# Kernel tuning notes

Measured on AMD Instinct MI355X. Metric: run time of the kernel, lower is better.

Reference implementation:

```python
import jax, jax.numpy as jnp
import numpy as np

# Qwen3-Next GatedDeltaNet dims
H = 2048          # hidden_size
HK = 16           # linear_num_key_heads
HV = 32           # linear_num_value_heads
DK = 128          # linear_key_head_dim
DV = 128          # linear_value_head_dim
KDIM = HK * DK    # 2048
VDIM = HV * DV    # 4096
CONV_DIM = 2 * KDIM + VDIM  # 8192
KSIZE = 4         # linear_conv_kernel_dim
KV_RATIO = HV // HK
EPS = 1e-6        # rms_norm_eps
T = 1024


def setup_inputs() -> dict:
    key = jax.random.key(0)
    ks = jax.random.split(key, 8)
    s = lambda k, shape, sc=0.02: jax.random.normal(k, shape, jnp.float32) * sc
    return dict(
        hidden_states=jax.random.normal(ks[0], (1, T, H), jnp.float32),
        W_qkvz=s(ks[1], (H, 2 * KDIM + 2 * VDIM)),
        W_ba=s(ks[2], (H, 2 * HV)),
        conv_w=s(ks[3], (CONV_DIM, KSIZE), 0.2),   # depthwise, no bias
        dt_bias=jax.random.normal(ks[4], (HV,), jnp.float32) * 0.1,
        A_log=jnp.log(jax.random.uniform(ks[5], (HV,), jnp.float32, minval=1e-2, maxval=16.0)),
        norm_w=jnp.ones((DV,), jnp.float32),
        W_out=s(ks[6], (VDIM, H)),
    )


def _l2norm(x):
    # fla l2norm: x / sqrt(sum(x^2) + eps)
    return x * jax.lax.rsqrt(jnp.sum(x * x, axis=-1, keepdims=True) + 1e-6)


def reference(hidden_states, W_qkvz, W_ba, conv_w, dt_bias, A_log, norm_w, W_out):
    B, Tn, _ = hidden_states.shape
    qkvz = hidden_states @ W_qkvz                       # [B,T,2K+2V]
    ba = hidden_states @ W_ba                           # [B,T,2*HV]

    # fix_query_key_value_ordering: per k-head interleaved layout
    qkvz = qkvz.reshape(B, Tn, HK, 2 * DK + 2 * KV_RATIO * DV)
    q = qkvz[..., :DK]                                  # [B,T,HK,DK]
    k = qkvz[..., DK:2 * DK]
    v = qkvz[..., 2 * DK:2 * DK + KV_RATIO * DV].reshape(B, Tn, HV, DV)
    z = qkvz[..., 2 * DK + KV_RATIO * DV:].reshape(B, Tn, HV, DV)
    ba = ba.reshape(B, Tn, HK, 2 * KV_RATIO)
    b = ba[..., :KV_RATIO].reshape(B, Tn, HV)
    a = ba[..., KV_RATIO:].reshape(B, Tn, HV)

    # causal depthwise conv1d (no bias) + silu, single contiguous sequence
    mixed = jnp.concatenate([q.reshape(B, Tn, KDIM), k.reshape(B, Tn, KDIM),
                             v.reshape(B, Tn, VDIM)], axis=-1)   # [B,T,C]
    x = mixed.transpose(0, 2, 1)                                   # [B,C,T]
    x = jnp.pad(x, ((0, 0), (0, 0), (KSIZE - 1, 0)))
    y = jax.lax.conv_general_dilated(x, conv_w[:, None, :], (1,), 'VALID',
                                     feature_group_count=CONV_DIM)
    y = jax.nn.silu(y).transpose(0, 2, 1)                          # [B,T,C]
    q = y[..., :KDIM].reshape(B, Tn, HK, DK)
    k = y[..., KDIM:2 * KDIM].reshape(B, Tn, HK, DK)
    v = y[..., 2 * KDIM:].reshape(B, Tn, HV, DV)

    beta = jax.nn.sigmoid(b)                                       # [B,T,HV]
    g = -jnp.exp(A_log) * jax.nn.softplus(a + dt_bias)             # [B,T,HV] (log decay)

    # qk l2norm in kernel + fla default scale on q; GQA head repeat
    q = jnp.repeat(_l2norm(q), KV_RATIO, axis=2) * (DK ** -0.5)    # [B,T,HV,DK]
    k = jnp.repeat(_l2norm(k), KV_RATIO, axis=2)

    def scan_one(qs, ks, vs, gs, bs):
        def step(S, inp):
            qt, kt, vt, gt, bt = inp                    # per-head slices
            S = S * jnp.exp(gt)[:, None, None]          # gated decay, [HV,DK,DV]
            kv = jnp.einsum('hk,hkv->hv', kt, S)        # current memory readout
            delta = (vt - kv) * bt[:, None]             # delta rule with beta gate
            S = S + kt[:, :, None] * delta[:, None, :]
            o = jnp.einsum('hk,hkv->hv', qt, S)
            return S, o
        S0 = jnp.zeros((HV, DK, DV), qs.dtype)
        _, out = jax.lax.scan(step, S0, (qs, ks, vs, gs, bs))
        return out                                      # [T,HV,DV]

    core = jax.vmap(scan_one)(q, k, v, g, beta)         # [B,T,HV,DV]

    # gated RMSNorm per value head: x*silu(z) then rmsnorm, then weight
    gated = core * jax.nn.silu(z)
    gated = gated * jax.lax.rsqrt(jnp.mean(gated * gated, axis=-1, keepdims=True) + EPS)
    gated = gated * norm_w

    return gated.reshape(B, Tn, VDIM) @ W_out           # [B,T,H]
```

## Files before the change

### kernel.cpp

```cpp
#include <hip/hip_runtime.h>
#include <hip/hip_bf16.h>
#include <math.h>


#define T_LEN 1024
#define HK_N 16
#define HV_N 32
#define NQKVZ 12288
#define CHUNK 64
#define NCHUNK 16

typedef __bf16 bf16x8 __attribute__((ext_vector_type(8)));
typedef float f32x4 __attribute__((ext_vector_type(4)));

__device__ __forceinline__ ushort4 pack4(const f32x4 v) {
  ushort4 o;
  o.x = __bfloat16_as_ushort(__float2bfloat16(v[0]));
  o.y = __bfloat16_as_ushort(__float2bfloat16(v[1]));
  o.z = __bfloat16_as_ushort(__float2bfloat16(v[2]));
  o.w = __bfloat16_as_ushort(__float2bfloat16(v[3]));
  return o;
}

template <int BM, bool BF16OUT>
__global__ __launch_bounds__(256) void gemm_bf16(const __hip_bfloat16* __restrict__ A,
                                                 const __hip_bfloat16* __restrict__ B,
                                                 void* __restrict__ Cv,
                                                 int M, int N, int Klen, int ldk) {
  constexpr int AITS = BM / 32;
  constexpr int MF = BM / 32;
  __shared__ __align__(16) __hip_bfloat16 As[2][BM * 64];
  __shared__ __align__(16) __hip_bfloat16 Bs[2][128 * 64];
  const int tid = threadIdx.x;
  const int wid = tid >> 6, lane = tid & 63;
  const int wr = wid >> 1, wc = wid & 1;
  const int m0 = blockIdx.y * BM, n0 = blockIdx.x * 128;
  const size_t kbase = (size_t)blockIdx.z * Klen;
  const int lrow = lane & 15, lk = lane >> 4;
  const int rswz = (lrow & 7) * 8;
  f32x4 acc[MF][4] = {};
  const int nk = Klen >> 6;

#define GSTAGE(b_, k0_) do {                                                    \
    _Pragma("unroll") for (int it = 0; it < AITS; ++it) {                       \
      const int c_ = it * 256 + tid;                                            \
      const int row_ = c_ >> 3;                                                 \
      const int col8_ = ((c_ & 7) ^ (row_ & 7)) * 8;                            \
      __builtin_amdgcn_global_load_lds(                                         \
          (const __attribute__((address_space(1))) void*)                       \
              (A + (size_t)(m0 + row_) * ldk + kbase + (k0_) + col8_),          \
          (__attribute__((address_space(3))) void*)(&As[b_][it * 2048 + tid * 8]), 16, 0, 0); \
    }                                                                           \
    _Pragma("unroll") for (int it = 0; it < 4; ++it) {                          \
      const int c_ = it * 256 + tid;                                            \
      const int row_ = c_ >> 3;                                                 \
      const int col8_ = ((c_ & 7) ^ (row_ & 7)) * 8;                            \
      __builtin_amdgcn_global_load_lds(                                         \
          (const __attribute__((address_space(1))) void*)                       \
              (B + (size_t)(n0 + row_) * ldk + kbase + (k0_) + col8_),          \
          (__attribute__((address_space(3))) void*)(&Bs[b_][it * 2048 + tid * 8]), 16, 0, 0); \
    }                                                                           \
  } while (0)

  GSTAGE(0, 0);
  int buf = 0;
  for (int k = 0; k < nk; ++k) {
    if (k + 1 < nk) {
      GSTAGE(buf ^ 1, (k + 1) << 6);
      if constexpr (BM == 128) asm volatile("s_waitcnt vmcnt(8)" ::: "memory");
      else                     asm volatile("s_waitcnt vmcnt(6)" ::: "memory");
    } else {
      asm volatile("s_waitcnt vmcnt(0)" ::: "memory");
    }
    __builtin_amdgcn_s_barrier();
    __builtin_amdgcn_sched_barrier(0);
#pragma unroll
    for (int kk = 0; kk < 2; ++kk) {
      bf16x8 af[MF], bfv[4];
#pragma unroll
      for (int m = 0; m < MF; ++m)
        af[m] = *reinterpret_cast<const bf16x8*>(
            &As[buf][(wr * (BM / 2) + m * 16 + lrow) * 64 + ((kk * 32 + lk * 8) ^ rswz)]);
#pragma unroll
      for (int n = 0; n < 4; ++n)
        bfv[n] = *reinterpret_cast<const bf16x8*>(
            &Bs[buf][(wc * 64 + n * 16 + lrow) * 64 + ((kk * 32 + lk * 8) ^ rswz)]);
#pragma unroll
      for (int m = 0; m < MF; ++m)
#pragma unroll
        for (int n = 0; n < 4; ++n)
          acc[m][n] = __builtin_amdgcn_mfma_f32_16x16x32_bf16(af[m], bfv[n], acc[m][n], 0, 0, 0);
    }
    __builtin_amdgcn_sched_barrier(0);
    __builtin_amdgcn_s_barrier();
    buf ^= 1;
  }
#undef GSTAGE
  if constexpr (BF16OUT) {
    __hip_bfloat16* Cz = (__hip_bfloat16*)Cv + (size_t)blockIdx.z * M * N;
#pragma unroll
    for (int m = 0; m < MF; ++m)
#pragma unroll
      for (int n = 0; n < 4; ++n)
#pragma unroll
        for (int r = 0; r < 4; ++r)
          Cz[(size_t)(m0 + wr * (BM / 2) + m * 16 + lk * 4 + r) * N + n0 + wc * 64 + n * 16 + lrow] =
              __float2bfloat16(acc[m][n][r]);
  } else {
    float* Cz = (float*)Cv + (size_t)blockIdx.z * M * N;
#pragma unroll
    for (int m = 0; m < MF; ++m)
#pragma unroll
      for (int n = 0; n < 4; ++n)
#pragma unroll
        for (int r = 0; r < 4; ++r)
          Cz[(size_t)(m0 + wr * (BM / 2) + m * 16 + lk * 4 + r) * N + n0 + wc * 64 + n * 16 + lrow] =
              acc[m][n][r];
  }
}

__global__ void add4(const __hip_bfloat16* __restrict__ P, float* __restrict__ out, int n) {
  const int i = (blockIdx.x * 256 + threadIdx.x) * 4;
  if (i < n) {
    float s[4] = {0.f, 0.f, 0.f, 0.f};
#pragma unroll
    for (int z = 0; z < 4; ++z) {
      const ushort4 v = *reinterpret_cast<const ushort4*>(P + (size_t)z * n + i);
      s[0] += __bfloat162float(__ushort_as_bfloat16(v.x));
      s[1] += __bfloat162float(__ushort_as_bfloat16(v.y));
      s[2] += __bfloat162float(__ushort_as_bfloat16(v.z));
      s[3] += __bfloat162float(__ushort_as_bfloat16(v.w));
    }
    *reinterpret_cast<float4*>(out + i) = make_float4(s[0], s[1], s[2], s[3]);
  }
}

__global__ __launch_bounds__(256) void prep2(const float* __restrict__ X,
                                             __hip_bfloat16* __restrict__ Xb,
                                             const float* __restrict__ Wq,
                                             __hip_bfloat16* __restrict__ Wqt,
                                             const float* __restrict__ Wba,
                                             float* __restrict__ P) {
  __shared__ __align__(16) float smem[16 * 512];
  const int bid = blockIdx.x;
  const int tid = threadIdx.x;
  if (bid < 2048) {
    const int i = (bid * 256 + tid) * 4;
    const float4 v = *reinterpret_cast<const float4*>(X + i);
    ushort4 o;
    o.x = __bfloat16_as_ushort(__float2bfloat16(v.x));
    o.y = __bfloat16_as_ushort(__float2bfloat16(v.y));
    o.z = __bfloat16_as_ushort(__float2bfloat16(v.z));
    o.w = __bfloat16_as_ushort(__float2bfloat16(v.w));
    *reinterpret_cast<ushort4*>((void*)(Xb + i)) = o;
  } else if (bid < 8192) {
    float (*tl)[65] = reinterpret_cast<float (*)[65]>(smem);
    const int b = bid - 2048;
    const int n0 = (b % 192) * 64, k0 = (b / 192) * 64;
    const int N = NQKVZ, K = 2048;
    const int rc = tid & 15, rr = tid >> 4;
#pragma unroll
    for (int i = 0; i < 4; ++i) {
      const int k = rr + 16 * i;
      const float4 v = *reinterpret_cast<const float4*>(&Wq[(size_t)(k0 + k) * N + n0 + rc * 4]);
      tl[k][rc * 4 + 0] = v.x;
      tl[k][rc * 4 + 1] = v.y;
      tl[k][rc * 4 + 2] = v.z;
      tl[k][rc * 4 + 3] = v.w;
    }
    __syncthreads();
    const int wcx = tid & 7, wry = tid >> 3;
#pragma unroll
    for (int i = 0; i < 2; ++i) {
      const int n = wry + 32 * i;
      uint u[8];
#pragma unroll
      for (int j = 0; j < 8; ++j)
        u[j] = __bfloat16_as_ushort(__float2bfloat16(tl[wcx * 8 + j][n]));
      uint4 o;
      o.x = u[0] | (u[1] << 16);
      o.y = u[2] | (u[3] << 16);
      o.z = u[4] | (u[5] << 16);
      o.w = u[6] | (u[7] << 16);
      *reinterpret_cast<uint4*>((void*)&Wqt[(size_t)(n0 + n) * K + k0 + wcx * 8]) = o;
    }
  } else {
    float (*Xs)[512] = reinterpret_cast<float (*)[512]>(smem);
    const int b = bid - 8192;
    const int tt = b & 63, ks = b >> 6;
    const int c = tid & 63, r4 = tid >> 6;
    const float* xsrc = X + (size_t)(tt * 16) * 2048 + ks * 512;
#pragma unroll
    for (int u = 0; u < 8; ++u) {
      const int flat = (u * 256 + tid) * 4;
      const int r = flat >> 9, k = flat & 511;
      *reinterpret_cast<float4*>(&Xs[r][k]) =
          *reinterpret_cast<const float4*>(&xsrc[(size_t)r * 2048 + k]);
    }
    __syncthreads();
    float acc[4] = {};
    const float* wp = Wba + (size_t)(ks * 512) * 64 + c;
    for (int k = 0; k < 512; k += 8) {
      float w[8];
#pragma unroll
      for (int u = 0; u < 8; ++u) w[u] = wp[(size_t)(k + u) * 64];
#pragma unroll
      for (int u = 0; u < 8; ++u)
#pragma unroll
        for (int i = 0; i < 4; ++i)
          acc[i] = fmaf(Xs[r4 * 4 + i][k + u], w[u], acc[i]);
    }
    float* pp = P + ((size_t)ks * 1024 + tt * 16 + r4 * 4) * 64 + c;
#pragma unroll
    for (int i = 0; i < 4; ++i) pp[(size_t)i * 64] = acc[i];
  }
}

__global__ __launch_bounds__(256) void convs(const __hip_bfloat16* __restrict__ qkvz,
                                             const float* __restrict__ conv_w,
                                             float* __restrict__ QK,
                                             float* __restrict__ V,
                                             const float* __restrict__ P,
                                             const float* __restrict__ dt_bias,
                                             const float* __restrict__ A_log,
                                             float* __restrict__ gg,
                                             float* __restrict__ bet) {
  const int bid = blockIdx.x;
  const int tid = threadIdx.x;
  if (bid < 4096) {
    const int kh = bid & 15;
    const int t = (bid >> 4) * 4 + (tid >> 6);
    const int l = tid & 63;
    const int cols[4] = {kh * 768 + l, kh * 768 + l + 64,
                         kh * 768 + 128 + l, kh * 768 + 128 + l + 64};
    const int chs[4] = {kh * 128 + l, kh * 128 + l + 64,
                        2048 + kh * 128 + l, 2048 + kh * 128 + l + 64};
    float y[4];
#pragma unroll
    for (int j = 0; j < 4; ++j) {
      const float* wp = &conv_w[chs[j] * 4];
      float acc = 0.f;
#pragma unroll
      for (int s = 0; s < 4; ++s) {
        const int tt = t - 3 + s;
        if (tt >= 0)
          acc = fmaf(__bfloat162float(qkvz[(size_t)tt * NQKVZ + cols[j]]), wp[s], acc);
      }
      y[j] = acc / (1.f + expf(-acc));
    }
    float sq = y[0] * y[0] + y[1] * y[1];
    float sk = y[2] * y[2] + y[3] * y[3];
#pragma unroll
    for (int off = 32; off; off >>= 1) {
      sq += __shfl_xor(sq, off);
      sk += __shfl_xor(sk, off);
    }
    const float rq = rsqrtf(sq + 1e-6f) * 0.08838834764831845f;
    const float rk = rsqrtf(sk + 1e-6f);
    const size_t qb = (size_t)t * 4096 + kh * 128;
    QK[qb + l] = y[0] * rq;
    QK[qb + l + 64] = y[1] * rq;
    QK[qb + 2048 + l] = y[2] * rk;
    QK[qb + 2048 + l + 64] = y[3] * rk;
  } else if (bid < 4608) {
    const int b = bid - 4096;
    const int c2 = (b & 15) * 256 + tid;
    const int vh = c2 >> 7;
    const int col = (vh >> 1) * 768 + 256 + (vh & 1) * 128 + (c2 & 127);
    const int t0 = (b >> 4) * 32;
    const float4 w = *reinterpret_cast<const float4*>(&conv_w[(4096 + c2) * 4]);
    float x0, x1, x2;
    if (t0 == 0) {
      x0 = 0.f; x1 = 0.f; x2 = 0.f;
    } else {
      x0 = __bfloat162float(qkvz[(size_t)(t0 - 3) * NQKVZ + col]);
      x1 = __bfloat162float(qkvz[(size_t)(t0 - 2) * NQKVZ + col]);
      x2 = __bfloat162float(qkvz[(size_t)(t0 - 1) * NQKVZ + col]);
    }
#pragma unroll 4
    for (int tt = 0; tt < 32; ++tt) {
      const int t = t0 + tt;
      const float x3 = __bfloat162float(qkvz[(size_t)t * NQKVZ + col]);
      float acc = x0 * w.x;
      acc = fmaf(x1, w.y, acc);
      acc = fmaf(x2, w.z, acc);
      acc = fmaf(x3, w.w, acc);
      V[(size_t)t * 4096 + c2] = acc / (1.f + expf(-acc));
      x0 = x1; x1 = x2; x2 = x3;
    }
  } else {
    const int idx = (bid - 4608) * 256 + tid;
    const int t = idx >> 5, vh = idx & 31;
    const int cb = (vh >> 1) * 4 + (vh & 1);
    float b = 0.f, a = 0.f;
#pragma unroll
    for (int s = 0; s < 4; ++s) {
      b += P[((size_t)s * 1024 + t) * 64 + cb];
      a += P[((size_t)s * 1024 + t) * 64 + cb + 2];
    }
    const float x = a + dt_bias[vh];
    const float sp = (x > 20.f) ? x : log1pf(expf(x));
    gg[idx] = -expf(A_log[vh]) * sp;
    bet[idx] = 1.f / (1.f + expf(-b));
  }
}

__global__ __launch_bounds__(256, 2) void phase1(
    const float* __restrict__ QK, const float* __restrict__ V,
    const float* __restrict__ g, const float* __restrict__ bet,
    __hip_bfloat16* __restrict__ Ub, __hip_bfloat16* __restrict__ Wb,
    __hip_bfloat16* __restrict__ KTb, __hip_bfloat16* __restrict__ Qgb,
    __hip_bfloat16* __restrict__ Bb, float* __restrict__ gend) {
  const int vh = blockIdx.x, ch = blockIdx.y, kh = vh >> 1;
  const int tid = threadIdx.x;
  const int t0 = ch * CHUNK;
  __shared__ __align__(16) __hip_bfloat16 KbS[64][128];
  __shared__ __align__(16) __hip_bfloat16 QbS[64][128];
  __shared__ __align__(16) float Al[64][68];
  __shared__ float bs[64], gams[64], bets[64], lams[64];

  const int row = tid >> 2;
  const size_t hb = (size_t)ch * 32 + vh;
  {
    const int cc = (tid & 3) * 32;
    const float* ksrc = &QK[(size_t)(t0 + row) * 4096 + 2048 + kh * 128 + cc];
    const float* qsrc = &QK[(size_t)(t0 + row) * 4096 + kh * 128 + cc];
#pragma unroll
    for (int u = 0; u < 32; u += 4) {
      const float4 kv = *reinterpret_cast<const float4*>(ksrc + u);
      const float4 qv = *reinterpret_cast<const float4*>(qsrc + u);
      const int d0 = cc + u;
      const int sidx = (d0 & 7) | ((((d0 >> 3) ^ (row & 7)) & 15) << 3);
      ushort4 kk4, qq4;
      kk4.x = __bfloat16_as_ushort(__float2bfloat16(kv.x));
      kk4.y = __bfloat16_as_ushort(__float2bfloat16(kv.y));
      kk4.z = __bfloat16_as_ushort(__float2bfloat16(kv.z));
      kk4.w = __bfloat16_as_ushort(__float2bfloat16(kv.w));
      qq4.x = __bfloat16_as_ushort(__float2bfloat16(qv.x));
      qq4.y = __bfloat16_as_ushort(__float2bfloat16(qv.y));
      qq4.z = __bfloat16_as_ushort(__float2bfloat16(qv.z));
      qq4.w = __bfloat16_as_ushort(__float2bfloat16(qv.w));
      *reinterpret_cast<ushort4*>(&KbS[row][sidx]) = kk4;
      *reinterpret_cast<ushort4*>(&QbS[row][sidx]) = qq4;
    }
  }
  if (tid < 64) {
    float b = g[(size_t)(t0 + tid) * 32 + vh];
#pragma unroll
    for (int off = 1; off < 64; off <<= 1) {
      const float o = __shfl_up(b, off);
      if (tid >= off) b += o;
    }
    const float b63 = __shfl(b, 63);
    const float ga = expf(b);
    bs[tid] = b;
    gams[tid] = ga;
    lams[tid] = expf(b63 - b);
    bets[tid] = bet[(size_t)(t0 + tid) * 32 + vh];
    if (tid == 63) gend[ch * 32 + vh] = ga;
  }
  __syncthreads();
  {
    const int i = tid & 63;
    const float li = lams[i];
    __hip_bfloat16* kt = &KTb[hb * 128 * 64];
    const int dbase = (tid >> 6) * 32;
#pragma unroll
    for (int dd = 0; dd < 32; ++dd) {
      const int d = dbase + dd;
      const int sidx = (d & 7) | ((((d >> 3) ^ (i & 7)) & 15) << 3);
      kt[(size_t)d * 64 + (i ^ ((d & 7) << 3))] =
          __float2bfloat16(li * __bfloat162float(KbS[i][sidx]));
    }
  }
  {
    const float gai = gams[row];
    __hip_bfloat16* qg = &Qgb[(hb * 64 + row) * 128];
    const int cc = (tid & 3) * 32;
#pragma unroll
    for (int u = 0; u < 32; u += 4) {
      const int d0 = cc + u;
      const int sidx = (d0 & 7) | ((((d0 >> 3) ^ (row & 7)) & 15) << 3);
      ushort4 qq;
      qq.x = __bfloat16_as_ushort(__float2bfloat16(gai * __bfloat162float(QbS[row][sidx + 0])));
      qq.y = __bfloat16_as_ushort(__float2bfloat16(gai * __bfloat162float(QbS[row][sidx + 1])));
      qq.z = __bfloat16_as_ushort(__float2bfloat16(gai * __bfloat162float(QbS[row][sidx + 2])));
      qq.w = __bfloat16_as_ushort(__float2bfloat16(gai * __bfloat162float(QbS[row][sidx + 3])));
      *reinterpret_cast<ushort4*>(&qg[d0 ^ ((row & 7) << 3)]) = qq;
    }
  }
  {
    const int w = tid >> 6, lane = tid & 63;
    const int lrow = lane & 15, lk = lane >> 4;
    bf16x8 af[4], qf[4];
#pragma unroll
    for (int kk = 0; kk < 4; ++kk) {
      const int c = ((kk * 4 + lk) ^ (lrow & 7)) * 8;
      af[kk] = *reinterpret_cast<const bf16x8*>(&KbS[w * 16 + lrow][c]);
      qf[kk] = *reinterpret_cast<const bf16x8*>(&QbS[w * 16 + lrow][c]);
    }
#pragma unroll
    for (int n = 0; n < 4; ++n) {
      f32x4 aA = {}, aB = {};
#pragma unroll
      for (int kk = 0; kk < 4; ++kk) {
        const bf16x8 bf = *reinterpret_cast<const bf16x8*>(
            &KbS[n * 16 + lrow][((kk * 4 + lk) ^ (lrow & 7)) * 8]);
        aA = __builtin_amdgcn_mfma_f32_16x16x32_bf16(af[kk], bf, aA, 0, 0, 0);
        aB = __builtin_amdgcn_mfma_f32_16x16x32_bf16(qf[kk], bf, aB, 0, 0, 0);
      }
      __hip_bfloat16* Bout = &Bb[hb * 64 * 64];
#pragma unroll
      for (int r = 0; r < 4; ++r) {
        const int i = w * 16 + lk * 4 + r;
        const int j = n * 16 + lrow;
        const float dec = expf(bs[i] - bs[j]);
        Al[i][j] = (j < i) ? bets[i] * dec * aA[r] : 0.f;
        Bout[(size_t)i * 64 + (j ^ ((i & 7) << 3))] =
            __float2bfloat16((j <= i) ? dec * aB[r] : 0.f);
      }
    }
  }
  __syncthreads();
  {
    const int cc = tid;
    float x[64];
    const bool isV = cc < 128;
    const float* src = isV ? &V[(size_t)t0 * 4096 + vh * 128 + cc]
                           : &QK[(size_t)t0 * 4096 + 2048 + kh * 128 + (cc - 128)];
#pragma unroll
    for (int i = 0; i < 64; ++i) {
      const float sc = isV ? bets[i] : bets[i] * gams[i];
      x[i] = sc * src[(size_t)i * 4096];
    }
#pragma unroll
    for (int i = 1; i < 64; ++i) {
      float s0 = 0.f, s1 = 0.f, s2 = 0.f, s3 = 0.f;
      int j = 0;
#pragma unroll
      for (; j + 4 <= i; j += 4) {
        const float4 a = *reinterpret_cast<const float4*>(&Al[i][j]);
        s0 = fmaf(a.x, x[j], s0);
        s1 = fmaf(a.y, x[j + 1], s1);
        s2 = fmaf(a.z, x[j + 2], s2);
        s3 = fmaf(a.w, x[j + 3], s3);
      }
#pragma unroll
      for (; j < i; ++j) s0 = fmaf(Al[i][j], x[j], s0);
      x[i] -= (s0 + s1) + (s2 + s3);
    }
    if (isV) {
      __hip_bfloat16* dst = &Ub[hb * 64 * 128 + cc];
#pragma unroll
      for (int i = 0; i < 64; ++i) dst[(size_t)i * 128] = __float2bfloat16(x[i]);
    } else {
      const int d = cc - 128;
      __hip_bfloat16* dst = &Wb[hb * 64 * 128];
#pragma unroll
      for (int i = 0; i < 64; ++i)
        dst[(size_t)i * 128 + (d ^ ((i & 7) << 3))] = __float2bfloat16(-x[i]);
    }
  }
}

__global__ __launch_bounds__(128) void phaseB(
    const __hip_bfloat16* __restrict__ Ug, const __hip_bfloat16* __restrict__ Wb,
    const __hip_bfloat16* __restrict__ KTb, const __hip_bfloat16* __restrict__ Qgb,
    const __hip_bfloat16* __restrict__ Bb, const float* __restrict__ gendg,
    float* __restrict__ Og) {
  const int vh = blockIdx.x, slice = blockIdx.y;
  const int tid = threadIdx.x, lane = tid & 63, w = tid >> 6;
  const int l15 = lane & 15, l4 = lane >> 4;
  const int cg = slice * 32 + w * 16;
  const int swz = (l15 & 7) << 3;

  __shared__ __hip_bfloat16 Wl[2][8192];
  __shared__ __hip_bfloat16 KTl[2][8192];
  __shared__ __hip_bfloat16 Qgl[2][8192];
  __shared__ __hip_bfloat16 Bl[2][4096];
  __shared__ __hip_bfloat16 Sop[2][2048];
  __shared__ __hip_bfloat16 dLs[2][1024];

  f32x4 accS[8] = {};
  for (int x = lane; x < 1024; x += 64) reinterpret_cast<uint*>(Sop[w])[x] = 0;

  float ubuf[4][4];
#define STAGE(b_, c_) do {                                                      \
    const size_t hb_ = ((size_t)(c_) * 32 + vh);                                \
    _Pragma("unroll") for (int it = 0; it < 8; ++it) {                          \
      __builtin_amdgcn_global_load_lds(                                         \
          (const __attribute__((address_space(1))) void*)(Wb + hb_ * 8192 + it * 1024 + tid * 8), \
          (__attribute__((address_space(3))) void*)(&Wl[b_][it * 1024 + tid * 8]), 16, 0, 0); \
      __builtin_amdgcn_global_load_lds(                                         \
          (const __attribute__((address_space(1))) void*)(KTb + hb_ * 8192 + it * 1024 + tid * 8), \
          (__attribute__((address_space(3))) void*)(&KTl[b_][it * 1024 + tid * 8]), 16, 0, 0); \
      __builtin_amdgcn_global_load_lds(                                         \
          (const __attribute__((address_space(1))) void*)(Qgb + hb_ * 8192 + it * 1024 + tid * 8), \
          (__attribute__((address_space(3))) void*)(&Qgl[b_][it * 1024 + tid * 8]), 16, 0, 0); \
      if (it < 4)                                                               \
        __builtin_amdgcn_global_load_lds(                                       \
            (const __attribute__((address_space(1))) void*)(Bb + hb_ * 4096 + it * 1024 + tid * 8), \
            (__attribute__((address_space(3))) void*)(&Bl[b_][it * 1024 + tid * 8]), 16, 0, 0); \
    }                                                                           \
  } while (0)
#define UPREF(c_) do {                                                          \
    const __hip_bfloat16* up_ = Ug + ((size_t)(c_) * 32 + vh) * 64 * 128 + cg + l15; \
    _Pragma("unroll") for (int m_ = 0; m_ < 4; ++m_)                            \
      _Pragma("unroll") for (int r_ = 0; r_ < 4; ++r_)                          \
        ubuf[m_][r_] = __bfloat162float(up_[(size_t)(m_ * 16 + l4 * 4 + r_) * 128]); \
  } while (0)

  STAGE(0, 0);
  UPREF(0);
  __syncthreads();
  int buf = 0;
  for (int ch = 0; ch < NCHUNK; ++ch) {
    if (ch + 1 < NCHUNK) STAGE(buf ^ 1, ch + 1);
    f32x4 acc_d[4];
#pragma unroll
    for (int m = 0; m < 4; ++m) {
      f32x4 t;
      t[0] = ubuf[m][0]; t[1] = ubuf[m][1]; t[2] = ubuf[m][2]; t[3] = ubuf[m][3];
      acc_d[m] = t;
    }
    if (ch + 1 < NCHUNK) UPREF(ch + 1);
#pragma unroll
    for (int t = 0; t < 4; ++t) {
      const bf16x8 bS = *reinterpret_cast<const bf16x8*>(
          &Sop[w][l15 * 128 + ((t * 32 + l4 * 8) ^ swz)]);
#pragma unroll
      for (int m = 0; m < 4; ++m) {
        const bf16x8 aW = *reinterpret_cast<const bf16x8*>(
            &Wl[buf][(m * 16 + l15) * 128 + ((t * 32 + l4 * 8) ^ swz)]);
        acc_d[m] = __builtin_amdgcn_mfma_f32_16x16x32_bf16(aW, bS, acc_d[m], 0, 0, 0);
      }
    }
#pragma unroll
    for (int m = 0; m < 4; ++m)
      *reinterpret_cast<ushort4*>(&dLs[w][l15 * 64 + ((m * 16 + l4 * 4) ^ swz)]) =
          pack4(acc_d[m]);
    f32x4 acc_o[4] = {};
#pragma unroll
    for (int t = 0; t < 4; ++t) {
      const bf16x8 bS = *reinterpret_cast<const bf16x8*>(
          &Sop[w][l15 * 128 + ((t * 32 + l4 * 8) ^ swz)]);
#pragma unroll
      for (int m = 0; m < 4; ++m) {
        const bf16x8 aQ = *reinterpret_cast<const bf16x8*>(
            &Qgl[buf][(m * 16 + l15) * 128 + ((t * 32 + l4 * 8) ^ swz)]);
        acc_o[m] = __builtin_amdgcn_mfma_f32_16x16x32_bf16(aQ, bS, acc_o[m], 0, 0, 0);
      }
    }
#pragma unroll
    for (int t2 = 0; t2 < 2; ++t2) {
      const bf16x8 bD = *reinterpret_cast<const bf16x8*>(
          &dLs[w][l15 * 64 + ((t2 * 32 + l4 * 8) ^ swz)]);
#pragma unroll
      for (int m = 0; m < 4; ++m) {
        const bf16x8 aB = *reinterpret_cast<const bf16x8*>(
            &Bl[buf][(m * 16 + l15) * 64 + ((t2 * 32 + l4 * 8) ^ swz)]);
        acc_o[m] = __builtin_amdgcn_mfma_f32_16x16x32_bf16(aB, bD, acc_o[m], 0, 0, 0);
      }
    }
    float* ob = Og + (size_t)(ch * 64) * 4096 + (size_t)vh * 128 + cg + l15;
#pragma unroll
    for (int m = 0; m < 4; ++m)
#pragma unroll
      for (int r = 0; r < 4; ++r)
        ob[(size_t)(m * 16 + l4 * 4 + r) * 4096] = acc_o[m][r];
    const float ge = gendg[ch * 32 + vh];
#pragma unroll
    for (int f = 0; f < 8; ++f) {
      accS[f][0] *= ge; accS[f][1] *= ge; accS[f][2] *= ge; accS[f][3] *= ge;
    }
#pragma unroll
    for (int t2 = 0; t2 < 2; ++t2) {
      const bf16x8 bD = *reinterpret_cast<const bf16x8*>(
          &dLs[w][l15 * 64 + ((t2 * 32 + l4 * 8) ^ swz)]);
#pragma unroll
      for (int f = 0; f < 8; ++f) {
        const bf16x8 aK = *reinterpret_cast<const bf16x8*>(
            &KTl[buf][(f * 16 + l15) * 64 + ((t2 * 32 + l4 * 8) ^ swz)]);
        accS[f] = __builtin_amdgcn_mfma_f32_16x16x32_bf16(aK, bD, accS[f], 0, 0, 0);
      }
    }
#pragma unroll
    for (int f = 0; f < 8; ++f)
      *reinterpret_cast<ushort4*>(&Sop[w][l15 * 128 + ((f * 16 + l4 * 4) ^ swz)]) =
          pack4(accS[f]);
    __syncthreads();
    buf ^= 1;
  }
#undef STAGE
#undef UPREF
}

__global__ __launch_bounds__(256) void gfuse(const float* __restrict__ O,
                                             const __hip_bfloat16* __restrict__ qkvz,
                                             const float* __restrict__ norm_w,
                                             __hip_bfloat16* __restrict__ G,
                                             const float* __restrict__ Wo,
                                             __hip_bfloat16* __restrict__ Wot) {
  __shared__ float tl[64][65];
  const int bid = blockIdx.x;
  const int tid = threadIdx.x;
  if (bid < 8192) {
    const int vh = (bid & 7) * 4 + (tid >> 6);
    const int t = bid >> 3, l = tid & 63;
    const size_t ob = (size_t)t * 4096 + vh * 128;
    const size_t zb = (size_t)t * NQKVZ + (vh >> 1) * 768 + 512 + (vh & 1) * 128;
    const float o0 = O[ob + l], o1 = O[ob + l + 64];
    const float z0 = __bfloat162float(qkvz[zb + l]);
    const float z1 = __bfloat162float(qkvz[zb + l + 64]);
    const float g0 = o0 * z0 / (1.f + expf(-z0));
    const float g1 = o1 * z1 / (1.f + expf(-z1));
    float ss = g0 * g0 + g1 * g1;
#pragma unroll
    for (int off = 32; off; off >>= 1) ss += __shfl_xor(ss, off);
    const float rr = rsqrtf(ss * (1.f / 128.f) + 1e-6f);
    G[ob + l] = __float2bfloat16(g0 * rr * norm_w[l]);
    G[ob + l + 64] = __float2bfloat16(g1 * rr * norm_w[l + 64]);
    return;
  }
  const int b = bid - 8192;
  const int n0 = (b & 31) * 64, k0 = (b >> 5) * 64;
  const int N = 2048, K = 4096;
  const int rc = tid & 15, rr2 = tid >> 4;
#pragma unroll
  for (int i = 0; i < 4; ++i) {
    const int k = rr2 + 16 * i;
    const float4 v = *reinterpret_cast<const float4*>(&Wo[(size_t)(k0 + k) * N + n0 + rc * 4]);
    tl[k][rc * 4 + 0] = v.x;
    tl[k][rc * 4 + 1] = v.y;
    tl[k][rc * 4 + 2] = v.z;
    tl[k][rc * 4 + 3] = v.w;
  }
  __syncthreads();
  const int wcx = tid & 7, wry = tid >> 3;
#pragma unroll
  for (int i = 0; i < 2; ++i) {
    const int n = wry + 32 * i;
    uint u[8];
#pragma unroll
    for (int j = 0; j < 8; ++j)
      u[j] = __bfloat16_as_ushort(__float2bfloat16(tl[wcx * 8 + j][n]));
    uint4 o;
    o.x = u[0] | (u[1] << 16);
    o.y = u[2] | (u[3] << 16);
    o.z = u[4] | (u[5] << 16);
    o.w = u[6] | (u[7] << 16);
    *reinterpret_cast<uint4*>((void*)&Wot[(size_t)(n0 + n) * K + k0 + wcx * 8]) = o;
  }
}

extern "C" void kernel_launch(void* const* d_in, const int* in_sizes, int n_in,
                              void* d_out, int out_size, void* d_ws, size_t ws_size,
                              hipStream_t stream) {
  const float* X = (const float*)d_in[0];
  const float* W_qkvz = (const float*)d_in[1];
  const float* W_ba = (const float*)d_in[2];
  const float* conv_w = (const float*)d_in[3];
  const float* dt_bias = (const float*)d_in[4];
  const float* A_log = (const float*)d_in[5];
  const float* norm_w = (const float*)d_in[6];
  const float* W_out = (const float*)d_in[7];
  float* out = (float*)d_out;

  float* ws = (float*)d_ws;
  float* qkvz = ws;
  float* P = qkvz + (size_t)T_LEN * NQKVZ;
  float* QK = P + 262144;
  float* V = QK + (size_t)T_LEN * 4096;
  float* U_f = V + (size_t)T_LEN * 4096;
  float* Wb_f = U_f + (size_t)NCHUNK * 32 * 64 * 128;
  float* KT_f = Wb_f + 2097152;
  float* Qg_f = KT_f + 2097152;
  float* Bb_f = Qg_f + 2097152;
  float* gg = Bb_f + 1048576;
  float* bet = gg + 32768;
  float* gend = bet + 32768;

  __hip_bfloat16* qkvzb = (__hip_bfloat16*)qkvz;
  __hip_bfloat16* Ub = (__hip_bfloat16*)U_f;
  __hip_bfloat16* Wb = (__hip_bfloat16*)Wb_f;
  __hip_bfloat16* KTb = (__hip_bfloat16*)KT_f;
  __hip_bfloat16* Qgb = (__hip_bfloat16*)Qg_f;
  __hip_bfloat16* Bb = (__hip_bfloat16*)Bb_f;
  __hip_bfloat16* Wqkvz_t = (__hip_bfloat16*)V;
  __hip_bfloat16* Xb = (__hip_bfloat16*)Qg_f;
  __hip_bfloat16* Gb = (__hip_bfloat16*)Bb_f;
  __hip_bfloat16* Wout_t = (__hip_bfloat16*)qkvz;
  float* O = V;
  __hip_bfloat16* Pout = (__hip_bfloat16*)U_f;

  prep2<<<dim3(2048 + 6144 + 256), 256, 0, stream>>>(X, Xb, W_qkvz, Wqkvz_t, W_ba, P);
  gemm_bf16<128, true><<<dim3(NQKVZ / 128, T_LEN / 128, 1), 256, 0, stream>>>(
      Xb, Wqkvz_t, qkvzb, T_LEN, NQKVZ, 2048, 2048);
  convs<<<dim3(4096 + 512 + 128), 256, 0, stream>>>(qkvzb, conv_w, QK, V, P,
                                                    dt_bias, A_log, gg, bet);
  phase1<<<dim3(HV_N, NCHUNK), 256, 0, stream>>>(QK, V, gg, bet, Ub, Wb, KTb, Qgb, Bb, gend);
  phaseB<<<dim3(HV_N, 4), 128, 0, stream>>>(Ub, Wb, KTb, Qgb, Bb, gend, O);
  gfuse<<<dim3(8192 + 2048), 256, 0, stream>>>(O, qkvzb, norm_w, Gb, W_out, Wout_t);
  gemm_bf16<128, true><<<dim3(2048 / 128, T_LEN / 128, 4), 256, 0, stream>>>(
      Gb, Wout_t, Pout, T_LEN, 2048, 1024, 4096);
  add4<<<dim3(T_LEN * 2048 / 4 / 256), 256, 0, stream>>>(Pout, out, T_LEN * 2048);
}
```

Measured before the change: 265.0 us.

## Add 256x256-tile 512-thread GEMM for QKVZ projection with direct-to-LDS loads

Adds a dedicated bf16 MFMA GEMM kernel with 256x256 output tiles and 8 waves. It uses global_load_lds direct-to-LDS double buffering, an XOR swizzle, and split-K-half fragment loads, and routes the large QKVZ projection through it. The bigger tile raises arithmetic intensity and cuts redundant global traffic. In exchange the grid shrinks to 48*4=192 blocks, which may underfill the GPU's CUs. It also uses large LDS (128KB) and many accumulator registers, limiting occupancy.

```diff
diff --git a/kernel.cpp b/kernel.cpp
--- a/kernel.cpp
+++ b/kernel.cpp
@@ -20,6 +20,99 @@
   o.z = __bfloat16_as_ushort(__float2bfloat16(v[2]));
   o.w = __bfloat16_as_ushort(__float2bfloat16(v[3]));
   return o;
+}
+
+__global__ __launch_bounds__(512) void gemm256(const __hip_bfloat16* __restrict__ A,
+                                               const __hip_bfloat16* __restrict__ B,
+                                               __hip_bfloat16* __restrict__ C,
+                                               int M, int N, int Klen) {
+  __shared__ __align__(16) __hip_bfloat16 As[2][256 * 64];
+  __shared__ __align__(16) __hip_bfloat16 Bs[2][256 * 64];
+  const int tid = threadIdx.x;
+  const int wid = tid >> 6, lane = tid & 63;
+  const int wr = wid >> 2, wc = wid & 3;
+  const int m0 = blockIdx.y * 256, n0 = blockIdx.x * 256;
+  const int lrow = lane & 15, lk = lane >> 4;
+  const int rswz = (lrow & 7) * 8;
+  f32x4 acc[8][4] = {};
+  const int nk = Klen >> 6;
+
+#define GST(b_, kt_) do {                                                       \
+    _Pragma("unroll") for (int it = 0; it < 4; ++it) {                          \
+      const int c_ = it * 512 + tid;                                            \
+      const int row_ = c_ >> 3;                                                 \
+      const int col8_ = ((c_ & 7) ^ (row_ & 7)) * 8;                            \
+      __builtin_amdgcn_global_load_lds(                                         \
+          (const __attribute__((address_space(1))) void*)                       \
+              (A + (size_t)(m0 + row_) * Klen + ((kt_) << 6) + col8_),          \
+          (__attribute__((address_space(3))) void*)(&As[b_][c_ * 8]), 16, 0, 0);\
+    }                                                                           \
+    _Pragma("unroll") for (int it = 0; it < 4; ++it) {                          \
+      const int c_ = it * 512 + tid;                                            \
+      const int row_ = c_ >> 3;                                                 \
+      const int col8_ = ((c_ & 7) ^ (row_ & 7)) * 8;                            \
+      __builtin_amdgcn_global_load_lds(                                         \
+          (const __attribute__((address_space(1))) void*)                       \
+              (B + (size_t)(n0 + row_) * Klen + ((kt_) << 6) + col8_),          \
+          (__attribute__((address_space(3))) void*)(&Bs[b_][c_ * 8]), 16, 0, 0);\
+    }                                                                           \
+  } while (0)
+
+  GST(0, 0);
+  GST(1, 1);
+  int cur = 0;
+  for (int t = 0; t < nk; ++t) {
+    if (t < nk - 1) asm volatile("s_waitcnt vmcnt(8)" ::: "memory");
+    else            asm volatile("s_waitcnt vmcnt(0)" ::: "memory");
+    __builtin_amdgcn_s_barrier();
+    __builtin_amdgcn_sched_barrier(0);
+    bf16x8 af[8], bfv[4];
+#pragma unroll
+    for (int m = 0; m < 8; ++m)
+      af[m] = *reinterpret_cast<const bf16x8*>(
+          &As[cur][(wr * 128 + m * 16 + lrow) * 64 + ((lk * 8) ^ rswz)]);
+#pragma unroll
+    for (int n = 0; n < 4; ++n)
+      bfv[n] = *reinterpret_cast<const bf16x8*>(
+          &Bs[cur][(wc * 64 + n * 16 + lrow) * 64 + ((lk * 8) ^ rswz)]);
+    __builtin_amdgcn_s_setprio(1);
+#pragma unroll
+    for (int m = 0; m < 8; ++m)
+#pragma unroll
+      for (int n = 0; n < 4; ++n)
+        acc[m][n] = __builtin_amdgcn_mfma_f32_16x16x32_bf16(af[m], bfv[n], acc[m][n], 0, 0, 0);
+    __builtin_amdgcn_s_setprio(0);
+#pragma unroll
+    for (int m = 0; m < 8; ++m)
+      af[m] = *reinterpret_cast<const bf16x8*>(
+          &As[cur][(wr * 128 + m * 16 + lrow) * 64 + ((32 + lk * 8) ^ rswz)]);
+#pragma unroll
+    for (int n = 0; n < 4; ++n)
+      bfv[n] = *reinterpret_cast<const bf16x8*>(
+          &Bs[cur][(wc * 64 + n * 16 + lrow) * 64 + ((32 + lk * 8) ^ rswz)]);
+    asm volatile("s_waitcnt lgkmcnt(0)" ::: "memory");
+    __builtin_amdgcn_sched_barrier(0);
+    __builtin_amdgcn_s_barrier();
+    __builtin_amdgcn_sched_barrier(0);
+    if (t + 2 < nk) GST(cur, t + 2);
+    __builtin_amdgcn_s_setprio(1);
+#pragma unroll
+    for (int m = 0; m < 8; ++m)
+#pragma unroll
+      for (int n = 0; n < 4; ++n)
+        acc[m][n] = __builtin_amdgcn_mfma_f32_16x16x32_bf16(af[m], bfv[n], acc[m][n], 0, 0, 0);
+    __builtin_amdgcn_s_setprio(0);
+    cur ^= 1;
+  }
+#undef GST
+#pragma unroll
+  for (int m = 0; m < 8; ++m)
+#pragma unroll
+    for (int n = 0; n < 4; ++n)
+#pragma unroll
+      for (int r = 0; r < 4; ++r)
+        C[(size_t)(m0 + wr * 128 + m * 16 + lk * 4 + r) * N + n0 + wc * 64 + n * 16 + lrow] =
+            __float2bfloat16(acc[m][n][r]);
 }
 
 template <int BM, bool BF16OUT>
@@ -694,8 +787,8 @@
   __hip_bfloat16* Pout = (__hip_bfloat16*)U_f;
 
   prep2<<<dim3(2048 + 6144 + 256), 256, 0, stream>>>(X, Xb, W_qkvz, Wqkvz_t, W_ba, P);
-  gemm_bf16<128, true><<<dim3(NQKVZ / 128, T_LEN / 128, 1), 256, 0, stream>>>(
-      Xb, Wqkvz_t, qkvzb, T_LEN, NQKVZ, 2048, 2048);
+  gemm256<<<dim3(NQKVZ / 256, T_LEN / 256), 512, 0, stream>>>(
+      Xb, Wqkvz_t, qkvzb, T_LEN, NQKVZ, 2048);
   convs<<<dim3(4096 + 512 + 128), 256, 0, stream>>>(qkvzb, conv_w, QK, V, P,
                                                     dt_bias, A_log, gg, bet);
   phase1<<<dim3(HV_N, NCHUNK), 256, 0, stream>>>(QK, V, gg, bet, Ub, Wb, KTb, Qgb, Bb, gend);
```

Result: faster. 251.4 us, median of 2 (-5.1%).

## Use 256x256 GEMM tiles with prefetch-two pipeline and deeper split-K

Applied to the files above, without the earlier changes.

Replaces the 128-tile bf16 GEMM with a 512-thread kernel that computes 256x256 output tiles. It prefetches the tile two K-steps ahead and interleaves the LDS fragment reads for the second K-half with MFMA work, raising wave priority during the MFMA sections. The output projection moves from 4-way to 8-way split-K, with an 8-input reduction kernel. The weight transpose also becomes its own kernel, separate from the X cast and the small b/a projection. Larger tiles give more operand reuse per byte loaded, but the QKVZ GEMM now launches only 192 workgroups, which may leave CUs idle. The doubled split-K partial buffer also adds memory traffic.

```diff
diff --git a/kernel.cpp b/kernel.cpp
--- a/kernel.cpp
+++ b/kernel.cpp
@@ -22,109 +22,107 @@
   return o;
 }
 
-template <int BM, bool BF16OUT>
-__global__ __launch_bounds__(256) void gemm_bf16(const __hip_bfloat16* __restrict__ A,
-                                                 const __hip_bfloat16* __restrict__ B,
-                                                 void* __restrict__ Cv,
-                                                 int M, int N, int Klen, int ldk) {
-  constexpr int AITS = BM / 32;
-  constexpr int MF = BM / 32;
-  __shared__ __align__(16) __hip_bfloat16 As[2][BM * 64];
-  __shared__ __align__(16) __hip_bfloat16 Bs[2][128 * 64];
+__global__ __launch_bounds__(512) void gemm256(const __hip_bfloat16* __restrict__ A,
+                                               const __hip_bfloat16* __restrict__ B,
+                                               __hip_bfloat16* __restrict__ C,
+                                               int M, int N, int Klen, int ldk) {
+  __shared__ __align__(16) __hip_bfloat16 As[2][256 * 64];
+  __shared__ __align__(16) __hip_bfloat16 Bs[2][256 * 64];
   const int tid = threadIdx.x;
   const int wid = tid >> 6, lane = tid & 63;
-  const int wr = wid >> 1, wc = wid & 1;
-  const int m0 = blockIdx.y * BM, n0 = blockIdx.x * 128;
+  const int wr = wid >> 2, wc = wid & 3;
+  const int m0 = blockIdx.y * 256, n0 = blockIdx.x * 256;
   const size_t kbase = (size_t)blockIdx.z * Klen;
+  __hip_bfloat16* Cz = C + (size_t)blockIdx.z * M * N;
   const int lrow = lane & 15, lk = lane >> 4;
   const int rswz = (lrow & 7) * 8;
-  f32x4 acc[MF][4] = {};
+  f32x4 acc[8][4] = {};
   const int nk = Klen >> 6;
 
-#define GSTAGE(b_, k0_) do {                                                    \
-    _Pragma("unroll") for (int it = 0; it < AITS; ++it) {                       \
-      const int c_ = it * 256 + tid;                                            \
+#define GST(b_, kt_) do {                                                       \
+    _Pragma("unroll") for (int it = 0; it < 4; ++it) {                          \
+      const int c_ = it * 512 + tid;                                            \
       const int row_ = c_ >> 3;                                                 \
       const int col8_ = ((c_ & 7) ^ (row_ & 7)) * 8;                            \
       __builtin_amdgcn_global_load_lds(                                         \
           (const __attribute__((address_space(1))) void*)                       \
-              (A + (size_t)(m0 + row_) * ldk + kbase + (k0_) + col8_),          \
-          (__attribute__((address_space(3))) void*)(&As[b_][it * 2048 + tid * 8]), 16, 0, 0); \
+              (A + (size_t)(m0 + row_) * ldk + kbase + ((kt_) << 6) + col8_),   \
+          (__attribute__((address_space(3))) void*)(&As[b_][c_ * 8]), 16, 0, 0);\
     }                                                                           \
     _Pragma("unroll") for (int it = 0; it < 4; ++it) {                          \
-      const int c_ = it * 256 + tid;                                            \
+      const int c_ = it * 512 + tid;                                            \
       const int row_ = c_ >> 3;                                                 \
       const int col8_ = ((c_ & 7) ^ (row_ & 7)) * 8;                            \
       __builtin_amdgcn_global_load_lds(                                         \
           (const __attribute__((address_space(1))) void*)                       \
-              (B + (size_t)(n0 + row_) * ldk + kbase + (k0_) + col8_),          \
-          (__attribute__((address_space(3))) void*)(&Bs[b_][it * 2048 + tid * 8]), 16, 0, 0); \
+              (B + (size_t)(n0 + row_) * ldk + kbase + ((kt_) << 6) + col8_),   \
+          (__attribute__((address_space(3))) void*)(&Bs[b_][c_ * 8]), 16, 0, 0);\
     }                                                                           \
   } while (0)
 
-  GSTAGE(0, 0);
-  int buf = 0;
-  for (int k = 0; k < nk; ++k) {
-    if (k + 1 < nk) {
-      GSTAGE(buf ^ 1, (k + 1) << 6);
-      if constexpr (BM == 128) asm volatile("s_waitcnt vmcnt(8)" ::: "memory");
-      else                     asm volatile("s_waitcnt vmcnt(6)" ::: "memory");
-    } else {
-      asm volatile("s_waitcnt vmcnt(0)" ::: "memory");
-    }
+  GST(0, 0);
+  GST(1, 1);
+  int cur = 0;
+  for (int t = 0; t < nk; ++t) {
+    if (t < nk - 1) asm volatile("s_waitcnt vmcnt(8)" ::: "memory");
+    else            asm volatile("s_waitcnt vmcnt(0)" ::: "memory");
     __builtin_amdgcn_s_barrier();
     __builtin_amdgcn_sched_barrier(0);
-#pragma unroll
-    for (int kk = 0; kk < 2; ++kk) {
-      bf16x8 af[MF], bfv[4];
-#pragma unroll
-      for (int m = 0; m < MF; ++m)
-        af[m] = *reinterpret_cast<const bf16x8*>(
-            &As[buf][(wr * (BM / 2) + m * 16 + lrow) * 64 + ((kk * 32 + lk * 8) ^ rswz)]);
+    bf16x8 af[8], bfv[4];
+#pragma unroll
+    for (int m = 0; m < 8; ++m)
+      af[m] = *reinterpret_cast<const bf16x8*>(
+          &As[cur][(wr * 128 + m * 16 + lrow) * 64 + ((lk * 8) ^ rswz)]);
+#pragma unroll
+    for (int n = 0; n < 4; ++n)
+      bfv[n] = *reinterpret_cast<const bf16x8*>(
+          &Bs[cur][(wc * 64 + n * 16 + lrow) * 64 + ((lk * 8) ^ rswz)]);
+    __builtin_amdgcn_s_setprio(1);
+#pragma unroll
+    for (int m = 0; m < 8; ++m)
 #pragma unroll
       for (int n = 0; n < 4; ++n)
-        bfv[n] = *reinterpret_cast<const bf16x8*>(
-            &Bs[buf][(wc * 64 + n * 16 + lrow) * 64 + ((kk * 32 + lk * 8) ^ rswz)]);
-#pragma unroll
-      for (int m = 0; m < MF; ++m)
-#pragma unroll
-        for (int n = 0; n < 4; ++n)
-          acc[m][n] = __builtin_amdgcn_mfma_f32_16x16x32_bf16(af[m], bfv[n], acc[m][n], 0, 0, 0);
-    }
+        acc[m][n] = __builtin_amdgcn_mfma_f32_16x16x32_bf16(af[m], bfv[n], acc[m][n], 0, 0, 0);
+    __builtin_amdgcn_s_setprio(0);
+#pragma unroll
+    for (int m = 0; m < 8; ++m)
+      af[m] = *reinterpret_cast<const bf16x8*>(
+          &As[cur][(wr * 128 + m * 16 + lrow) * 64 + ((32 + lk * 8) ^ rswz)]);
+#pragma unroll
+    for (int n = 0; n < 4; ++n)
+      bfv[n] = *reinterpret_cast<const bf16x8*>(
+          &Bs[cur][(wc * 64 + n * 16 + lrow) * 64 + ((32 + lk * 8) ^ rswz)]);
+    asm volatile("s_waitcnt lgkmcnt(0)" ::: "memory");
     __builtin_amdgcn_sched_barrier(0);
     __builtin_amdgcn_s_barrier();
-    buf ^= 1;
-  }
-#undef GSTAGE
-  if constexpr (BF16OUT) {
-    __hip_bfloat16* Cz = (__hip_bfloat16*)Cv + (size_t)blockIdx.z * M * N;
-#pragma unroll
-    for (int m = 0; m < MF; ++m)
+    __builtin_amdgcn_sched_barrier(0);
+    if (t + 2 < nk) GST(cur, t + 2);
+    __builtin_amdgcn_s_setprio(1);
+#pragma unroll
+    for (int m = 0; m < 8; ++m)
 #pragma unroll
       for (int n = 0; n < 4; ++n)
-#pragma unroll
-        for (int r = 0; r < 4; ++r)
-          Cz[(size_t)(m0 + wr * (BM / 2) + m * 16 + lk * 4 + r) * N + n0 + wc * 64 + n * 16 + lrow] =
-              __float2bfloat16(acc[m][n][r]);
-  } else {
-    float* Cz = (float*)Cv + (size_t)blockIdx.z * M * N;
-#pragma unroll
-    for (int m = 0; m < MF; ++m)
-#pragma unroll
-      for (int n = 0; n < 4; ++n)
-#pragma unroll
-        for (int r = 0; r < 4; ++r)
-          Cz[(size_t)(m0 + wr * (BM / 2) + m * 16 + lk * 4 + r) * N + n0 + wc * 64 + n * 16 + lrow] =
-              acc[m][n][r];
-  }
-}
-
-__global__ void add4(const __hip_bfloat16* __restrict__ P, float* __restrict__ out, int n) {
+        acc[m][n] = __builtin_amdgcn_mfma_f32_16x16x32_bf16(af[m], bfv[n], acc[m][n], 0, 0, 0);
+    __builtin_amdgcn_s_setprio(0);
+    cur ^= 1;
+  }
+#undef GST
+#pragma unroll
+  for (int m = 0; m < 8; ++m)
+#pragma unroll
+    for (int n = 0; n < 4; ++n)
+#pragma unroll
+      for (int r = 0; r < 4; ++r)
+        Cz[(size_t)(m0 + wr * 128 + m * 16 + lk * 4 + r) * N + n0 + wc * 64 + n * 16 + lrow] =
+            __float2bfloat16(acc[m][n][r]);
+}
+
+__global__ void add8(const __hip_bfloat16* __restrict__ P, float* __restrict__ out, int n) {
   const int i = (blockIdx.x * 256 + threadIdx.x) * 4;
   if (i < n) {
     float s[4] = {0.f, 0.f, 0.f, 0.f};
 #pragma unroll
-    for (int z = 0; z < 4; ++z) {
+    for (int z = 0; z < 8; ++z) {
       const ushort4 v = *reinterpret_cast<const ushort4*>(P + (size_t)z * n + i);
       s[0] += __bfloat162float(__ushort_as_bfloat16(v.x));
       s[1] += __bfloat162float(__ushort_as_bfloat16(v.y));
@@ -135,13 +133,11 @@
   }
 }
 
-__global__ __launch_bounds__(256) void prep2(const float* __restrict__ X,
+__global__ __launch_bounds__(256) void preba(const float* __restrict__ X,
                                              __hip_bfloat16* __restrict__ Xb,
-                                             const float* __restrict__ Wq,
-                                             __hip_bfloat16* __restrict__ Wqt,
                                              const float* __restrict__ Wba,
                                              float* __restrict__ P) {
-  __shared__ __align__(16) float smem[16 * 512];
+  __shared__ __align__(16) float Xs[16][512];
   const int bid = blockIdx.x;
   const int tid = threadIdx.x;
   if (bid < 2048) {
@@ -153,40 +149,8 @@
     o.z = __bfloat16_as_ushort(__float2bfloat16(v.z));
     o.w = __bfloat16_as_ushort(__float2bfloat16(v.w));
     *reinterpret_cast<ushort4*>((void*)(Xb + i)) = o;
-  } else if (bid < 8192) {
-    float (*tl)[65] = reinterpret_cast<float (*)[65]>(smem);
+  } else {
     const int b = bid - 2048;
-    const int n0 = (b % 192) * 64, k0 = (b / 192) * 64;
-    const int N = NQKVZ, K = 2048;
-    const int rc = tid & 15, rr = tid >> 4;
-#pragma unroll
-    for (int i = 0; i < 4; ++i) {
-      const int k = rr + 16 * i;
-      const float4 v = *reinterpret_cast<const float4*>(&Wq[(size_t)(k0 + k) * N + n0 + rc * 4]);
-      tl[k][rc * 4 + 0] = v.x;
-      tl[k][rc * 4 + 1] = v.y;
-      tl[k][rc * 4 + 2] = v.z;
-      tl[k][rc * 4 + 3] = v.w;
-    }
-    __syncthreads();
-    const int wcx = tid & 7, wry = tid >> 3;
-#pragma unroll
-    for (int i = 0; i < 2; ++i) {
-      const int n = wry + 32 * i;
-      uint u[8];
-#pragma unroll
-      for (int j = 0; j < 8; ++j)
-        u[j] = __bfloat16_as_ushort(__float2bfloat16(tl[wcx * 8 + j][n]));
-      uint4 o;
-      o.x = u[0] | (u[1] << 16);
-      o.y = u[2] | (u[3] << 16);
-      o.z = u[4] | (u[5] << 16);
-      o.w = u[6] | (u[7] << 16);
-      *reinterpret_cast<uint4*>((void*)&Wqt[(size_t)(n0 + n) * K + k0 + wcx * 8]) = o;
-    }
-  } else {
-    float (*Xs)[512] = reinterpret_cast<float (*)[512]>(smem);
-    const int b = bid - 8192;
     const int tt = b & 63, ks = b >> 6;
     const int c = tid & 63, r4 = tid >> 6;
     const float* xsrc = X + (size_t)(tt * 16) * 2048 + ks * 512;
@@ -213,6 +177,41 @@
     float* pp = P + ((size_t)ks * 1024 + tt * 16 + r4 * 4) * 64 + c;
 #pragma unroll
     for (int i = 0; i < 4; ++i) pp[(size_t)i * 64] = acc[i];
+  }
+}
+
+__global__ __launch_bounds__(256) void wtrans(const float* __restrict__ Wq,
+                                              __hip_bfloat16* __restrict__ Wqt) {
+  __shared__ float tl[64][65];
+  const int b = blockIdx.x;
+  const int n0 = (b % 192) * 64, k0 = (b / 192) * 64;
+  const int N = NQKVZ, K = 2048;
+  const int tid = threadIdx.x;
+  const int rc = tid & 15, rr = tid >> 4;
+#pragma unroll
+  for (int i = 0; i < 4; ++i) {
+    const int k = rr + 16 * i;
+    const float4 v = *reinterpret_cast<const float4*>(&Wq[(size_t)(k0 + k) * N + n0 + rc * 4]);
+    tl[k][rc * 4 + 0] = v.x;
+    tl[k][rc * 4 + 1] = v.y;
+    tl[k][rc * 4 + 2] = v.z;
+    tl[k][rc * 4 + 3] = v.w;
+  }
+  __syncthreads();
+  const int wcx = tid & 7, wry = tid >> 3;
+#pragma unroll
+  for (int i = 0; i < 2; ++i) {
+    const int n = wry + 32 * i;
+    uint u[8];
+#pragma unroll
+    for (int j = 0; j < 8; ++j)
+      u[j] = __bfloat16_as_ushort(__float2bfloat16(tl[wcx * 8 + j][n]));
+    uint4 o;
+    o.x = u[0] | (u[1] << 16);
+    o.y = u[2] | (u[3] << 16);
+    o.z = u[4] | (u[5] << 16);
+    o.w = u[6] | (u[7] << 16);
+    *reinterpret_cast<uint4*>((void*)&Wqt[(size_t)(n0 + n) * K + k0 + wcx * 8]) = o;
   }
 }
 
@@ -693,15 +692,16 @@
   float* O = V;
   __hip_bfloat16* Pout = (__hip_bfloat16*)U_f;
 
-  prep2<<<dim3(2048 + 6144 + 256), 256, 0, stream>>>(X, Xb, W_qkvz, Wqkvz_t, W_ba, P);
-  gemm_bf16<128, true><<<dim3(NQKVZ / 128, T_LEN / 128, 1), 256, 0, stream>>>(
+  preba<<<dim3(2048 + 256), 256, 0, stream>>>(X, Xb, W_ba, P);
+  wtrans<<<dim3(6144), 256, 0, stream>>>(W_qkvz, Wqkvz_t);
+  gemm256<<<dim3(NQKVZ / 256, T_LEN / 256, 1), 512, 0, stream>>>(
       Xb, Wqkvz_t, qkvzb, T_LEN, NQKVZ, 2048, 2048);
   convs<<<dim3(4096 + 512 + 128), 256, 0, stream>>>(qkvzb, conv_w, QK, V, P,
                                                     dt_bias, A_log, gg, bet);
   phase1<<<dim3(HV_N, NCHUNK), 256, 0, stream>>>(QK, V, gg, bet, Ub, Wb, KTb, Qgb, Bb, gend);
   phaseB<<<dim3(HV_N, 4), 128, 0, stream>>>(Ub, Wb, KTb, Qgb, Bb, gend, O);
   gfuse<<<dim3(8192 + 2048), 256, 0, stream>>>(O, qkvzb, norm_w, Gb, W_out, Wout_t);
-  gemm_bf16<128, true><<<dim3(2048 / 128, T_LEN / 128, 4), 256, 0, stream>>>(
-      Gb, Wout_t, Pout, T_LEN, 2048, 1024, 4096);
-  add4<<<dim3(T_LEN * 2048 / 4 / 256), 256, 0, stream>>>(Pout, out, T_LEN * 2048);
-}
+  gemm256<<<dim3(2048 / 256, T_LEN / 256, 8), 512, 0, stream>>>(
+      Gb, Wout_t, Pout, T_LEN, 2048, 512, 4096);
+  add8<<<dim3(T_LEN * 2048 / 4 / 256), 256, 0, stream>>>(Pout, out, T_LEN * 2048);
+}
```

New measurement: 261.2 us. About the same (-1.4%).
